# Performance work log

Hardware: AMD Instinct MI355X
Metric: run time of the kernel (lower is better)

Reference implementation:

```python
import jax, jax.numpy as jnp
import numpy as np

NUM_KEYS = 64

def setup_inputs() -> dict:
    key = jax.random.key(0)
    k1, k2 = jax.random.split(key)
    inputs = jax.random.randint(k1, (8, 4096, 1024), 0, NUM_KEYS, dtype=jnp.int32)
    # learned per-key bias (build() creates shape (num_keys,) for key_shape=[1])
    b = jax.random.normal(k2, (NUM_KEYS,), dtype=jnp.float32)
    # keys are sorted unique scalars (0..63), stored as float like the TF cast
    keys = jnp.arange(NUM_KEYS, dtype=jnp.float32)
    return {"inputs": inputs, "b": b, "keys": keys}


def reference(inputs, b, keys):
    # Original math: out = sum_k (inputs == keys[k]) * b[k], elementwise over inputs.
    # With unique sorted keys this is a gather: find the matching key index per
    # element and pick b there; elements matching no key contribute 0.
    # This avoids the O(num_keys * numel) broadcast blow-up of the TF graph.
    xf = inputs.astype(jnp.float32)
    K = keys.shape[0]
    idx = jnp.clip(jnp.searchsorted(keys, xf), 0, K - 1)  # [8,4096,1024]
    out = jnp.where(keys[idx] == xf, b[idx], jnp.float32(0.0))
    return out
```

## Files before the change

### kernel.cpp

```cpp
#include <hip/hip_runtime.h>

#define NKEYS 64
#define BATCH 8

typedef float vfloat4 __attribute__((ext_vector_type(4)));

__device__ __forceinline__ float bperm_f(int lane_idx, int src_i) {
    return __int_as_float(__builtin_amdgcn_ds_bpermute(lane_idx << 2, src_i));
}

__global__ __launch_bounds__(256) void sel_xform_kernel(
    const int4* __restrict__ in,
    const float* __restrict__ b,
    const float* __restrict__ keys,
    float* __restrict__ out,
    int nvec, int ntail, const int* __restrict__ in_tail, float* __restrict__ out_tail)
{
    __shared__ float t[NKEYS];
    const int tid  = threadIdx.x;
    const int lane = tid & 63;

    const float kv = keys[lane];
    const float bv = b[lane];

    const int base = blockIdx.x * (256 * BATCH) + tid;
    int4 v[BATCH];
    bool p[BATCH];
    #pragma unroll
    for (int j = 0; j < BATCH; ++j) {
        const int idx = base + j * 256;
        p[j] = idx < nvec;
        if (p[j]) v[j] = in[idx];
        else      v[j] = int4{0, 0, 0, 0};
    }

    const int   kv_i   = __float_as_int(kv);
    const float target = (float)lane;
    int pos = 0;
    #pragma unroll
    for (int s = 32; s >= 1; s >>= 1) {
        const float kc = bperm_f(pos + s - 1, kv_i);
        if (kc < target) pos += s;
    }
    const int posc = (pos > NKEYS - 1) ? (NKEYS - 1) : pos;
    const float kmatch = bperm_f(posc, kv_i);
    const float bval   = bperm_f(posc, __float_as_int(bv));
    const float tv     = (kmatch == target) ? bval : 0.0f;

    if (tid < NKEYS) t[tid] = tv;
    __syncthreads();

    #pragma unroll
    for (int j = 0; j < BATCH; ++j) {
        if (p[j]) {
            const int4 x = v[j];
            vfloat4 o;
            o.x = ((unsigned)x.x < NKEYS) ? t[x.x] : 0.0f;
            o.y = ((unsigned)x.y < NKEYS) ? t[x.y] : 0.0f;
            o.z = ((unsigned)x.z < NKEYS) ? t[x.z] : 0.0f;
            o.w = ((unsigned)x.w < NKEYS) ? t[x.w] : 0.0f;
            *(vfloat4*)(out + ((long)(base + j * 256) << 2)) = o;
        }
    }

    if (blockIdx.x == 0 && tid < ntail) {
        const float xf = (float)in_tail[tid];
        float r = 0.0f;
        for (int k = 0; k < NKEYS; ++k) r = (keys[k] == xf) ? b[k] : r;
        out_tail[tid] = r;
    }
}

extern "C" void kernel_launch(void* const* d_in, const int* in_sizes, int n_in,
                              void* d_out, int out_size, void* d_ws, size_t ws_size,
                              hipStream_t stream) {
    const int*   x    = (const int*)d_in[0];
    const float* b    = (const float*)d_in[1];
    const float* keys = (const float*)d_in[2];
    float* out = (float*)d_out;

    const int n     = in_sizes[0];
    const int nvec  = n >> 2;
    const int ntail = n & 3;

    int grid = (nvec + 2047) / 2048;
    if (grid < 1) grid = 1;

    sel_xform_kernel<<<grid, 256, 0, stream>>>(
        (const int4*)x, b, keys, out,
        nvec, ntail, x + (nvec << 2), out + (nvec << 2));
}
```

Before: 231.2 us.

## Use persistent grid-stride loop with per-wave LUT and nontemporal stores

Replaces the one-shot batch-of-8 loads per block with a fixed 2048-block persistent grid that walks the input in a grid-stride loop, prefetching the next int4 while processing the current one. Each wavefront builds its own 64-entry lookup table in shared memory, which removes the block-wide __syncthreads in favour of a wave-level fence. Output writes become nontemporal stores to avoid polluting cache. The trade-off is only one outstanding load per thread instead of eight, which may reduce memory-level parallelism on a bandwidth-bound kernel.

```diff
diff --git a/kernel.cpp b/kernel.cpp
--- a/kernel.cpp
+++ b/kernel.cpp
@@ -1,7 +1,6 @@
 #include <hip/hip_runtime.h>
 
 #define NKEYS 64
-#define BATCH 8
 
 typedef float vfloat4 __attribute__((ext_vector_type(4)));
 
@@ -16,24 +15,13 @@
     float* __restrict__ out,
     int nvec, int ntail, const int* __restrict__ in_tail, float* __restrict__ out_tail)
 {
-    __shared__ float t[NKEYS];
+    __shared__ float t[4][NKEYS];
     const int tid  = threadIdx.x;
     const int lane = tid & 63;
+    const int wv   = tid >> 6;
 
     const float kv = keys[lane];
     const float bv = b[lane];
-
-    const int base = blockIdx.x * (256 * BATCH) + tid;
-    int4 v[BATCH];
-    bool p[BATCH];
-    #pragma unroll
-    for (int j = 0; j < BATCH; ++j) {
-        const int idx = base + j * 256;
-        p[j] = idx < nvec;
-        if (p[j]) v[j] = in[idx];
-        else      v[j] = int4{0, 0, 0, 0};
-    }
-
     const int   kv_i   = __float_as_int(kv);
     const float target = (float)lane;
     int pos = 0;
@@ -45,21 +33,30 @@
     const int posc = (pos > NKEYS - 1) ? (NKEYS - 1) : pos;
     const float kmatch = bperm_f(posc, kv_i);
     const float bval   = bperm_f(posc, __float_as_int(bv));
-    const float tv     = (kmatch == target) ? bval : 0.0f;
+    t[wv][lane] = (kmatch == target) ? bval : 0.0f;
+    __threadfence_block();
 
-    if (tid < NKEYS) t[tid] = tv;
-    __syncthreads();
+    const float* __restrict__ tw = t[wv];
 
-    #pragma unroll
-    for (int j = 0; j < BATCH; ++j) {
-        if (p[j]) {
-            const int4 x = v[j];
+    int i = blockIdx.x * blockDim.x + tid;
+    const int stride = gridDim.x * blockDim.x;
+
+    if (i < nvec) {
+        int4 v = in[i];
+        for (;;) {
+            const int  inext = i + stride;
+            const bool more  = inext < nvec;
+            int4 vn;
+            if (more) vn = in[inext];
             vfloat4 o;
-            o.x = ((unsigned)x.x < NKEYS) ? t[x.x] : 0.0f;
-            o.y = ((unsigned)x.y < NKEYS) ? t[x.y] : 0.0f;
-            o.z = ((unsigned)x.z < NKEYS) ? t[x.z] : 0.0f;
-            o.w = ((unsigned)x.w < NKEYS) ? t[x.w] : 0.0f;
-            *(vfloat4*)(out + ((long)(base + j * 256) << 2)) = o;
+            o.x = ((unsigned)v.x < NKEYS) ? tw[v.x] : 0.0f;
+            o.y = ((unsigned)v.y < NKEYS) ? tw[v.y] : 0.0f;
+            o.z = ((unsigned)v.z < NKEYS) ? tw[v.z] : 0.0f;
+            o.w = ((unsigned)v.w < NKEYS) ? tw[v.w] : 0.0f;
+            __builtin_nontemporal_store(o, (vfloat4*)(out + ((long)i << 2)));
+            if (!more) break;
+            v = vn;
+            i = inext;
         }
     }
 
@@ -83,7 +80,9 @@
     const int nvec  = n >> 2;
     const int ntail = n & 3;
 
-    int grid = (nvec + 2047) / 2048;
+    int grid = 2048;
+    const int nvec_blocks = (nvec + 255) / 256;
+    if (grid > nvec_blocks) grid = nvec_blocks;
     if (grid < 1) grid = 1;
 
     sel_xform_kernel<<<grid, 256, 0, stream>>>(
```

Result: no change. 234.4 us (+1.4%).
